# Optimization experiments

Measured on AMD Instinct MI355X. Metric: run time of the kernel, lower is better.

## Reference

```python
import jax, jax.numpy as jnp
import numpy as np

B, N, D, H, F, K, L, V, E, C = 8, 256, 768, 8, 3072, 128, 8, 32, 1024, 2
HD = D // H
LN_EPS = 1e-3  # keras LayerNormalization default epsilon
GAUSS_A = (2.0 * 3.14159) ** 0.5  # constant from source


def _ln(x, g, b):
    m = jnp.mean(x, axis=-1, keepdims=True)
    v = jnp.mean((x - m) ** 2, axis=-1, keepdims=True)
    return (x - m) * jax.lax.rsqrt(v + LN_EPS) * g + b


def _gelu(x):
    return jax.nn.gelu(x, approximate=False)  # keras 'gelu' is exact


def setup_inputs() -> dict:
    key = jax.random.key(0)
    ks = iter(jax.random.split(key, 40))
    s = 0.02
    inp = {
        'dist': jax.random.uniform(next(ks), (B, N, N), jnp.float32) * 10.0,
        'tok_emb': jax.random.normal(next(ks), (V, D), jnp.float32) * s,
        'gmeans': jax.random.uniform(next(ks), (K,), jnp.float32) * 3.0,
        'gstds': jax.random.uniform(next(ks), (K,), jnp.float32) * 3.0,
        'gmul': jnp.ones((E, 1), jnp.float32),
        'gbias': jnp.zeros((E, 1), jnp.float32),
        'gp1w': jax.random.normal(next(ks), (K, K), jnp.float32) * s,
        'gp1b': jnp.zeros((K,), jnp.float32),
        'gp2w': jax.random.normal(next(ks), (K, H), jnp.float32) * s,
        'gp2b': jnp.zeros((H,), jnp.float32),
        'emb_ln_g': jnp.ones((D,), jnp.float32),
        'emb_ln_b': jnp.zeros((D,), jnp.float32),
        'Wq': jax.random.normal(next(ks), (L, D, D), jnp.float32) * s,
        'bq': jnp.zeros((L, D), jnp.float32),
        'Wo': jax.random.normal(next(ks), (L, D, D), jnp.float32) * s,
        'bo': jnp.zeros((L, D), jnp.float32),
        'ln1g': jnp.ones((L, D), jnp.float32),
        'ln1b': jnp.zeros((L, D), jnp.float32),
        'W1': jax.random.normal(next(ks), (L, D, F), jnp.float32) * s,
        'b1': jnp.zeros((L, F), jnp.float32),
        'W2': jax.random.normal(next(ks), (L, F, D), jnp.float32) * s,
        'b2': jnp.zeros((L, D), jnp.float32),
        'ln2g': jnp.ones((L, D), jnp.float32),
        'ln2b': jnp.zeros((L, D), jnp.float32),
        'fin_ln_g': jnp.ones((D,), jnp.float32),
        'fin_ln_b': jnp.zeros((D,), jnp.float32),
        'cls_w1': jax.random.normal(next(ks), (D, D), jnp.float32) * s,
        'cls_b1': jnp.zeros((D,), jnp.float32),
        'cls_w2': jax.random.normal(next(ks), (D, C), jnp.float32) * s,
        'cls_b2': jnp.zeros((C,), jnp.float32),
        'tokens': jax.random.randint(next(ks), (B, N), 0, V, jnp.int64),
        'edge_type': jax.random.randint(next(ks), (B, N, N), 0, E, jnp.int64),
    }
    return inp


def _forward(dist, tok_emb, gmeans, gstds, gmul, gbias, gp1w, gp1b, gp2w, gp2b,
             emb_ln_g, emb_ln_b, Wq, bq, Wo, bo, ln1g, ln1b, W1, b1, W2, b2,
             ln2g, ln2b, fin_ln_g, fin_ln_b, cls_w1, cls_b1, cls_w2, cls_b2,
             tokens, edge_type):
    # --- Gaussian pairwise bias ---
    mul = gmul[edge_type][..., 0]      # (B,N,N)
    add = gbias[edge_type][..., 0]     # (B,N,N)
    y = mul * dist + add               # (B,N,N)
    std = jnp.abs(gstds) + 1e-5        # (K,)
    g = jnp.exp(-0.5 * ((y[..., None] - gmeans) / std) ** 2) / (GAUSS_A * std)  # (B,N,N,K)
    pb = _gelu(g @ gp1w + gp1b) @ gp2w + gp2b   # (B,N,N,H)
    attn_bias = jnp.transpose(pb, (0, 3, 1, 2))  # (B,H,N,N)

    # --- encoder (pre-LN), NB: wq is shared for q/k/v as in source ---
    x = tok_emb[tokens]                # (B,N,D)
    x = _ln(x, emb_ln_g, emb_ln_b)
    scale = 1.0 / np.sqrt(HD).astype(np.float32)

    def split_heads(t):
        return t.reshape(B, N, H, HD).transpose(0, 2, 1, 3)  # (B,H,N,HD)

    for i in range(L):
        r = x
        h = _ln(x, ln1g[i], ln1b[i])
        q = split_heads((h @ Wq[i] + bq[i]) * scale)
        k = split_heads(h @ Wq[i] + bq[i])
        v = split_heads(h @ Wq[i] + bq[i])
        s = jnp.einsum('bhnd,bhmd->bhnm', q, k) + attn_bias
        p = jax.nn.softmax(s, axis=-1)
        o = jnp.einsum('bhnm,bhmd->bhnd', p, v)
        o = o.transpose(0, 2, 1, 3).reshape(B, N, D) @ Wo[i] + bo[i]
        x = o + r
        r = x
        h = _ln(x, ln2g[i], ln2b[i])
        x = _gelu(h @ W1[i] + b1[i]) @ W2[i] + b2[i] + r
    x = _ln(x, fin_ln_g, fin_ln_b)

    # --- classification head on CLS token ---
    cls = x[:, 0, :]
    return _gelu(cls @ cls_w1 + cls_b1) @ cls_w2 + cls_b2  # (B,C)


def reference(dist, tok_emb, gmeans, gstds, gmul, gbias, gp1w, gp1b, gp2w, gp2b,
              emb_ln_g, emb_ln_b, Wq, bq, Wo, bo, ln1g, ln1b, W1, b1, W2, b2,
              ln2g, ln2b, fin_ln_g, fin_ln_b, cls_w1, cls_b1, cls_w2, cls_b2,
              tokens, edge_type):
    return _forward(dist, tok_emb, gmeans, gstds, gmul, gbias, gp1w, gp1b, gp2w,
                    gp2b, emb_ln_g, emb_ln_b, Wq, bq, Wo, bo, ln1g, ln1b, W1, b1,
                    W2, b2, ln2g, ln2b, fin_ln_g, fin_ln_b, cls_w1, cls_b1,
                    cls_w2, cls_b2, tokens, edge_type)
```

## Files before the change

### kernel.cpp

```cpp
#include <hip/hip_runtime.h>
#include <hip/hip_bf16.h>
#include <math.h>


#define DEV_INLINE __device__ __forceinline__

typedef __attribute__((ext_vector_type(8))) short short8v;
typedef __attribute__((ext_vector_type(4))) short short4v;
typedef __attribute__((ext_vector_type(4))) float f32x4;

DEV_INLINE unsigned short f2bf(float f) {
  unsigned u = __float_as_uint(f);
  return (unsigned short)((u + 0x7fffu + ((u >> 16) & 1u)) >> 16);
}
DEV_INLINE unsigned short f2bf_hw(float f) {
  __hip_bfloat16 h = __float2bfloat16(f);
  unsigned short u; __builtin_memcpy(&u, &h, 2); return u;
}
DEV_INLINE float gelu_f(float v) {
  return 0.5f * v * (1.0f + erff(v * 0.70710678118654752f));
}
DEV_INLINE float gelu_tanh(float x) {
  float x2 = x * x;
  float t  = x * fmaf(0.044715f, x2, 1.0f);
  float a  = fminf(2.3022082f * t, 252.0f);
  float e  = __builtin_amdgcn_exp2f(a);
  return x * e * __frcp_rn(e + 1.0f);
}
DEV_INLINE f32x4 zero4() { f32x4 z; z[0]=0.f; z[1]=0.f; z[2]=0.f; z[3]=0.f; return z; }

__global__ __launch_bounds__(256) void k_cast_t(
    const float* __restrict__ W, unsigned short* __restrict__ Wt, int K, int N)
{
  __shared__ float s[64][68];
  const int tid = threadIdx.x;
  const size_t lay = (size_t)blockIdx.z * K * N;
  const int k0 = blockIdx.x * 64, n0 = blockIdx.y * 64;
  const int r = tid >> 4, c4 = (tid & 15) << 2;
  #pragma unroll
  for (int i = 0; i < 4; ++i)
    *(float4*)&s[r + i * 16][c4] =
        *(const float4*)(W + lay + (size_t)(k0 + r + i * 16) * N + n0 + c4);
  __syncthreads();
  const int n = tid & 63, kc = (tid >> 6) << 4;
  short8v v0, v1;
  #pragma unroll
  for (int j = 0; j < 8; ++j) v0[j] = (short)f2bf(s[kc + j][n]);
  #pragma unroll
  for (int j = 0; j < 8; ++j) v1[j] = (short)f2bf(s[kc + 8 + j][n]);
  unsigned short* dst = Wt + lay + (size_t)(n0 + n) * K + k0 + kc;
  *(short8v*)dst = v0;
  *(short8v*)(dst + 8) = v1;
}

__global__ __launch_bounds__(128) void k_cast_g1(
    const float* __restrict__ gp1w, const float* __restrict__ gstds,
    unsigned short* __restrict__ g1t)
{
  const int k = threadIdx.x;
  const int n = blockIdx.x;
  float sd = fabsf(gstds[k]) + 1e-5f;
  float coef = 0.39894268f / sd;
  g1t[n * 128 + k] = f2bf(coef * gp1w[k * 128 + n]);
}

template<int BM, int BN, int EPI>
__global__ __launch_bounds__(256) void k_gemm(
    const unsigned short* __restrict__ A, const unsigned short* __restrict__ Bt,
    const float* __restrict__ bias, const float* __restrict__ res,
    void* __restrict__ C, unsigned short* __restrict__ Vt, int N, int K)
{
  constexpr int MA = BM / 32;
  constexpr int NB = BN / 32;
  __shared__ __align__(16) unsigned short As[BM * 64];
  __shared__ __align__(16) unsigned short Bs[BN * 64];
  const int tid = threadIdx.x;
  const int l = tid & 63;
  const int w = tid >> 6, wr = w >> 1, wc = w & 1;
  const int row0 = blockIdx.x * BM, col0 = blockIdx.y * BN;
  const int NT = K >> 6;

  const int rA = tid >> 3;
  const int cs = (((tid & 7) * 16) ^ ((rA & 7) << 4)) >> 1;
  const unsigned short* pa = A + (size_t)(row0 + rA) * K + (tid & 7) * 8;
  const unsigned short* pb = Bt + (size_t)(col0 + rA) * K + (tid & 7) * 8;

  short8v ra[MA], rb[NB];
  #pragma unroll
  for (int i = 0; i < MA; ++i) ra[i] = *(const short8v*)(pa + (size_t)i * 32 * K);
  #pragma unroll
  for (int i = 0; i < NB; ++i) rb[i] = *(const short8v*)(pb + (size_t)i * 32 * K);

  f32x4 acc[MA][NB];
  #pragma unroll
  for (int mi = 0; mi < MA; ++mi)
    #pragma unroll
    for (int ni = 0; ni < NB; ++ni) acc[mi][ni] = zero4();

  for (int kt = 0; kt < NT; ++kt) {
    #pragma unroll
    for (int i = 0; i < MA; ++i) *(short8v*)&As[(rA + i * 32) * 64 + cs] = ra[i];
    #pragma unroll
    for (int i = 0; i < NB; ++i) *(short8v*)&Bs[(rA + i * 32) * 64 + cs] = rb[i];
    __syncthreads();
    if (kt + 1 < NT) {
      const unsigned short* qa = pa + (size_t)(kt + 1) * 64;
      const unsigned short* qb = pb + (size_t)(kt + 1) * 64;
      #pragma unroll
      for (int i = 0; i < MA; ++i) ra[i] = *(const short8v*)(qa + (size_t)i * 32 * K);
      #pragma unroll
      for (int i = 0; i < NB; ++i) rb[i] = *(const short8v*)(qb + (size_t)i * 32 * K);
    }
    #pragma unroll
    for (int kk = 0; kk < 2; ++kk) {
      short8v af[MA], bf_[NB];
      #pragma unroll
      for (int mi = 0; mi < MA; ++mi) {
        int rw = wr * (BM / 2) + mi * 16 + (l & 15);
        int kb = (kk * 64 + ((l >> 4) << 4)) ^ ((rw & 7) << 4);
        af[mi] = *(const short8v*)&As[rw * 64 + (kb >> 1)];
      }
      #pragma unroll
      for (int ni = 0; ni < NB; ++ni) {
        int rw = wc * (BN / 2) + ni * 16 + (l & 15);
        int kb = (kk * 64 + ((l >> 4) << 4)) ^ ((rw & 7) << 4);
        bf_[ni] = *(const short8v*)&Bs[rw * 64 + (kb >> 1)];
      }
      #pragma unroll
      for (int mi = 0; mi < MA; ++mi)
        #pragma unroll
        for (int ni = 0; ni < NB; ++ni)
          acc[mi][ni] = __builtin_amdgcn_mfma_f32_16x16x32_bf16(
              af[mi], bf_[ni], acc[mi][ni], 0, 0, 0);
    }
    __syncthreads();
  }

  const int cl = l & 15, rg = (l >> 4) << 2;
  #pragma unroll
  for (int mi = 0; mi < MA; ++mi) {
    #pragma unroll
    for (int ni = 0; ni < NB; ++ni) {
      const int colg = col0 + wc * (BN / 2) + ni * 16 + cl;
      const float bv = bias[colg];
      const size_t rbase = (size_t)(row0 + wr * (BM / 2) + mi * 16 + rg);
      if (EPI == 4) {
        short4v pk;
        #pragma unroll
        for (int r = 0; r < 4; ++r) {
          float v = acc[mi][ni][r] + bv;
          unsigned short bb = f2bf(v);
          ((unsigned short*)C)[(rbase + r) * N + colg] = bb;
          pk[r] = (short)bb;
        }
        const int hh = colg / 96, dd = colg - hh * 96;
        const int bb_ = (int)(rbase >> 8), tok = (int)(rbase & 255);
        *(short4v*)(Vt + ((size_t)((bb_ << 3) + hh) * 96 + dd) * 256 + tok) = pk;
      } else {
        #pragma unroll
        for (int r = 0; r < 4; ++r) {
          size_t off = (rbase + r) * N + colg;
          float v = acc[mi][ni][r] + bv;
          if (EPI == 0) ((unsigned short*)C)[off] = f2bf(v);
          if (EPI == 1) ((unsigned short*)C)[off] = f2bf(gelu_f(v));
          if (EPI == 2) ((float*)C)[off] = v + res[off];
        }
      }
    }
  }
}

__global__ __launch_bounds__(256) void k_gauss(
    const float* __restrict__ dist, const int* __restrict__ edge,
    const float* __restrict__ gmul, const float* __restrict__ gbias,
    const float* __restrict__ gmeans, const float* __restrict__ gstds,
    const unsigned short* __restrict__ gp1wt, const float* __restrict__ gp1b,
    const float* __restrict__ gp2w, const float* __restrict__ gp2b,
    float* __restrict__ bias_out)
{
  __shared__ float mean_s[128], c2_s[128], b1s[128];
  __shared__ float b2s[8];
  __shared__ __align__(16) unsigned short w2t[16 * 136];
  __shared__ __align__(16) unsigned short t1[4][2048];
  const int tid = threadIdx.x, l = tid & 63, w = tid >> 6;
  const int pos0 = blockIdx.x * 64;

  if (tid < 128) {
    float sd = fabsf(gstds[tid]) + 1e-5f;
    float inv = 1.0f / sd;
    mean_s[tid] = gmeans[tid];
    c2_s[tid] = -0.72134752f * inv * inv;
    b1s[tid] = gp1b[tid];
  }
  if (tid < 8) b2s[tid] = gp2b[tid];
  for (int i = tid; i < 2048; i += 256) {
    int hh = i & 15, k = i >> 4;
    w2t[hh * 136 + k] = (hh < 8) ? f2bf(gp2w[k * 8 + hh]) : (unsigned short)0;
  }
  __syncthreads();

  const int p = pos0 + w * 16 + (l & 15);
  const int et = edge[p];
  const float y = gmul[et] * dist[p] + gbias[et];

  short8v ga[4];
  #pragma unroll
  for (int ks = 0; ks < 4; ++ks) {
    #pragma unroll
    for (int j = 0; j < 8; ++j) {
      int k = ks * 32 + ((l >> 4) << 3) + j;
      float d = y - mean_s[k];
      ga[ks][j] = (short)f2bf_hw(__builtin_amdgcn_exp2f(c2_s[k] * d * d));
    }
  }
  f32x4 acc[8];
  #pragma unroll
  for (int n = 0; n < 8; ++n) {
    acc[n] = zero4();
    const unsigned short* bp = gp1wt + (size_t)(n * 16 + (l & 15)) * 128 + ((l >> 4) << 3);
    #pragma unroll
    for (int ks = 0; ks < 4; ++ks)
      acc[n] = __builtin_amdgcn_mfma_f32_16x16x32_bf16(
          ga[ks], *(const short8v*)(bp + ks * 32), acc[n], 0, 0, 0);
  }
  unsigned short* tw = t1[w];
  {
    const int rb = (l >> 4) << 2;
    #pragma unroll
    for (int n = 0; n < 8; ++n) {
      int col2 = (n * 16 + (l & 15)) * 2;
      float bb = b1s[n * 16 + (l & 15)];
      #pragma unroll
      for (int r = 0; r < 4; ++r) {
        int row = rb + r;
        int swz = ((row & 3) << 4) ^ ((row >> 2) << 5);
        tw[(row * 256 + (col2 ^ swz)) >> 1] = f2bf_hw(gelu_tanh(acc[n][r] + bb));
      }
    }
  }
  f32x4 o4 = zero4();
  {
    const int row = l & 15;
    const int swz = ((row & 3) << 4) ^ ((row >> 2) << 5);
    #pragma unroll
    for (int ks = 0; ks < 4; ++ks) {
      short8v af = *(const short8v*)&tw[(row * 256 + ((ks * 64 + ((l >> 4) << 4)) ^ swz)) >> 1];
      short8v bf_ = *(const short8v*)&w2t[(l & 15) * 136 + ks * 32 + ((l >> 4) << 3)];
      o4 = __builtin_amdgcn_mfma_f32_16x16x32_bf16(af, bf_, o4, 0, 0, 0);
    }
  }
  const int hh = l & 15;
  if (hh < 8) {
    int b = pos0 >> 16;
    int ij = (pos0 & 65535) + w * 16 + ((l >> 4) << 2);
    float4 vv;
    vv.x = o4[0] + b2s[hh]; vv.y = o4[1] + b2s[hh];
    vv.z = o4[2] + b2s[hh]; vv.w = o4[3] + b2s[hh];
    *(float4*)(bias_out + ((size_t)((b << 3) + hh) << 16) + ij) = vv;
  }
}

__global__ __launch_bounds__(256) void k_embed2(
    const float* __restrict__ emb, const int* __restrict__ tokens,
    const float* __restrict__ eg, const float* __restrict__ eb,
    const float* __restrict__ g1, const float* __restrict__ bp1,
    float* __restrict__ x, unsigned short* __restrict__ h)
{
  __shared__ float red[4], red2[4];
  const int t = threadIdx.x;
  const int row = blockIdx.x;
  const float* xr = emb + (size_t)tokens[row] * 768;
  float v0 = xr[t], v1 = xr[t + 256], v2 = xr[t + 512];
  float s = v0 + v1 + v2;
  #pragma unroll
  for (int o = 32; o; o >>= 1) s += __shfl_down(s, o);
  if ((t & 63) == 0) red[t >> 6] = s;
  __syncthreads();
  float mean = (red[0] + red[1] + red[2] + red[3]) * (1.0f / 768.0f);
  float d0 = v0 - mean, d1 = v1 - mean, d2 = v2 - mean;
  float q = d0 * d0 + d1 * d1 + d2 * d2;
  #pragma unroll
  for (int o = 32; o; o >>= 1) q += __shfl_down(q, o);
  if ((t & 63) == 0) red2[t >> 6] = q;
  __syncthreads();
  float rstd = rsqrtf((red2[0] + red2[1] + red2[2] + red2[3]) * (1.0f / 768.0f) + 1e-3f);
  float* outr = x + (size_t)row * 768;
  float y0 = d0 * rstd * eg[t]       + eb[t];
  float y1 = d1 * rstd * eg[t + 256] + eb[t + 256];
  float y2 = d2 * rstd * eg[t + 512] + eb[t + 512];
  outr[t] = y0; outr[t + 256] = y1; outr[t + 512] = y2;
  __syncthreads();
  s = y0 + y1 + y2;
  #pragma unroll
  for (int o = 32; o; o >>= 1) s += __shfl_down(s, o);
  if ((t & 63) == 0) red[t >> 6] = s;
  __syncthreads();
  mean = (red[0] + red[1] + red[2] + red[3]) * (1.0f / 768.0f);
  d0 = y0 - mean; d1 = y1 - mean; d2 = y2 - mean;
  q = d0 * d0 + d1 * d1 + d2 * d2;
  #pragma unroll
  for (int o = 32; o; o >>= 1) q += __shfl_down(q, o);
  if ((t & 63) == 0) red2[t >> 6] = q;
  __syncthreads();
  rstd = rsqrtf((red2[0] + red2[1] + red2[2] + red2[3]) * (1.0f / 768.0f) + 1e-3f);
  unsigned short* hr = h + (size_t)row * 768;
  hr[t]       = f2bf(d0 * rstd * g1[t]       + bp1[t]);
  hr[t + 256] = f2bf(d1 * rstd * g1[t + 256] + bp1[t + 256]);
  hr[t + 512] = f2bf(d2 * rstd * g1[t + 512] + bp1[t + 512]);
}

__global__ __launch_bounds__(256) void k_ln_bf(
    const float* __restrict__ in, const float* __restrict__ g,
    const float* __restrict__ bp, unsigned short* __restrict__ out)
{
  __shared__ float red[4], red2[4];
  const int t = threadIdx.x;
  const size_t base = (size_t)blockIdx.x * 768;
  const float* xr = in + base;
  float v0 = xr[t], v1 = xr[t + 256], v2 = xr[t + 512];
  float s = v0 + v1 + v2;
  #pragma unroll
  for (int o = 32; o; o >>= 1) s += __shfl_down(s, o);
  if ((t & 63) == 0) red[t >> 6] = s;
  __syncthreads();
  float mean = (red[0] + red[1] + red[2] + red[3]) * (1.0f / 768.0f);
  float d0 = v0 - mean, d1 = v1 - mean, d2 = v2 - mean;
  float q = d0 * d0 + d1 * d1 + d2 * d2;
  #pragma unroll
  for (int o = 32; o; o >>= 1) q += __shfl_down(q, o);
  if ((t & 63) == 0) red2[t >> 6] = q;
  __syncthreads();
  float rstd = rsqrtf((red2[0] + red2[1] + red2[2] + red2[3]) * (1.0f / 768.0f) + 1e-3f);
  unsigned short* outr = out + base;
  outr[t]       = f2bf(d0 * rstd * g[t]       + bp[t]);
  outr[t + 256] = f2bf(d1 * rstd * g[t + 256] + bp[t + 256]);
  outr[t + 512] = f2bf(d2 * rstd * g[t + 512] + bp[t + 512]);
}

__global__ __launch_bounds__(256) void k_attn(
    const unsigned short* __restrict__ P, const unsigned short* __restrict__ Vt,
    const float* __restrict__ bias, unsigned short* __restrict__ O)
{
  __shared__ __align__(16) unsigned short pl[4][4096];
  const int tid = threadIdx.x, l = tid & 63, w = tid >> 6;
  const int i0 = blockIdx.x << 6, bh = blockIdx.y, b = bh >> 3, hh = bh & 7;
  const unsigned short* Pb = P + (size_t)b * 196608 + hh * 96;

  short8v aq[3];
  const int rq = i0 + w * 16 + (l & 15);
  #pragma unroll
  for (int ks = 0; ks < 3; ++ks)
    aq[ks] = *(const short8v*)(Pb + (size_t)rq * 768 + ks * 32 + ((l >> 4) << 3));

  f32x4 acc[16];
  #pragma unroll
  for (int n = 0; n < 16; ++n) {
    acc[n] = zero4();
    const unsigned short* kp = Pb + (size_t)(n * 16 + (l & 15)) * 768 + ((l >> 4) << 3);
    #pragma unroll
    for (int ks = 0; ks < 3; ++ks)
      acc[n] = __builtin_amdgcn_mfma_f32_16x16x32_bf16(
          aq[ks], *(const short8v*)(kp + ks * 32), acc[n], 0, 0, 0);
  }

  const float scale = 0.10206207261596577f;
  float inv[4];
  unsigned short* plw = pl[w];
  const size_t brow = ((size_t)bh * 256 + i0 + w * 16 + ((l >> 4) << 2)) * 256 + (l & 15);
  #pragma unroll
  for (int r = 0; r < 4; ++r) {
    const float* bptr = bias + brow + (size_t)r * 256;
    float m = -1e30f;
    #pragma unroll
    for (int n = 0; n < 16; ++n) {
      float v = acc[n][r] * scale + bptr[n * 16];
      acc[n][r] = v;
      m = fmaxf(m, v);
    }
    m = fmaxf(m, __shfl_xor(m, 1)); m = fmaxf(m, __shfl_xor(m, 2));
    m = fmaxf(m, __shfl_xor(m, 4)); m = fmaxf(m, __shfl_xor(m, 8));
    const int rowL = ((l >> 4) << 2) + r;
    const int swz = ((rowL & 3) << 4) ^ ((rowL >> 2) << 5);
    const int cb = (l & 15) << 1;
    float s = 0.f;
    #pragma unroll
    for (int n = 0; n < 16; ++n) {
      float e = __expf(acc[n][r] - m);
      s += e;
      plw[(rowL * 512 + ((cb + (n << 5)) ^ swz)) >> 1] = f2bf_hw(e);
    }
    s += __shfl_xor(s, 1); s += __shfl_xor(s, 2);
    s += __shfl_xor(s, 4); s += __shfl_xor(s, 8);
    inv[r] = 1.0f / s;
  }

  const int rowA = l & 15;
  const int swzA = ((rowA & 3) << 4) ^ ((rowA >> 2) << 5);
  short8v pa[8];
  #pragma unroll
  for (int ks = 0; ks < 8; ++ks)
    pa[ks] = *(const short8v*)&plw[(rowA * 512 + ((ks * 64 + ((l >> 4) << 4)) ^ swzA)) >> 1];

  unsigned short* Ob = O + ((size_t)b * 256 + i0 + w * 16 + ((l >> 4) << 2)) * 768
                       + hh * 96 + (l & 15);
  #pragma unroll
  for (int n = 0; n < 6; ++n) {
    f32x4 a2 = zero4();
    const unsigned short* vb = Vt + ((size_t)bh * 96 + n * 16 + (l & 15)) * 256 + ((l >> 4) << 3);
    #pragma unroll
    for (int ks = 0; ks < 8; ++ks)
      a2 = __builtin_amdgcn_mfma_f32_16x16x32_bf16(
          pa[ks], *(const short8v*)(vb + ks * 32), a2, 0, 0, 0);
    #pragma unroll
    for (int r = 0; r < 4; ++r)
      Ob[(size_t)r * 768 + n * 16] = f2bf(a2[r] * inv[r]);
  }
}

__global__ __launch_bounds__(256) void k_cls_ln(
    const float* __restrict__ x, const float* __restrict__ fg,
    const float* __restrict__ fb, float* __restrict__ lnb)
{
  __shared__ float red[4], red2[4];
  const int t = threadIdx.x;
  const int b = blockIdx.x;
  const float* xr = x + (size_t)b * 196608;
  float v0 = xr[t], v1 = xr[t + 256], v2 = xr[t + 512];
  float s = v0 + v1 + v2;
  #pragma unroll
  for (int o = 32; o; o >>= 1) s += __shfl_down(s, o);
  if ((t & 63) == 0) red[t >> 6] = s;
  __syncthreads();
  float mean = (red[0] + red[1] + red[2] + red[3]) * (1.0f / 768.0f);
  float d0 = v0 - mean, d1 = v1 - mean, d2 = v2 - mean;
  float q = d0 * d0 + d1 * d1 + d2 * d2;
  #pragma unroll
  for (int o = 32; o; o >>= 1) q += __shfl_down(q, o);
  if ((t & 63) == 0) red2[t >> 6] = q;
  __syncthreads();
  float rstd = rsqrtf((red2[0] + red2[1] + red2[2] + red2[3]) * (1.0f / 768.0f) + 1e-3f);
  float* outr = lnb + b * 768;
  outr[t]       = d0 * rstd * fg[t]       + fb[t];
  outr[t + 256] = d1 * rstd * fg[t + 256] + fb[t + 256];
  outr[t + 512] = d2 * rstd * fg[t + 512] + fb[t + 512];
}

__global__ __launch_bounds__(256) void k_cls_mm(
    const float* __restrict__ lnb, const float* __restrict__ w1,
    const float* __restrict__ b1v, float* __restrict__ t1g)
{
  __shared__ float ln[768];
  const int t = threadIdx.x;
  const int b = blockIdx.x, c0 = blockIdx.y * 256;
  #pragma unroll
  for (int i = 0; i < 3; ++i) ln[t + i * 256] = lnb[b * 768 + t + i * 256];
  __syncthreads();
  float a = b1v[c0 + t];
  for (int d = 0; d < 768; ++d)
    a = fmaf(ln[d], w1[d * 768 + c0 + t], a);
  t1g[b * 768 + c0 + t] = gelu_f(a);
}

__global__ __launch_bounds__(256) void k_cls_out(
    const float* __restrict__ t1g, const float* __restrict__ w2,
    const float* __restrict__ b2v, float* __restrict__ out)
{
  __shared__ float r2[8];
  const int t = threadIdx.x;
  const int b = blockIdx.x;
  float p0 = 0.f, p1 = 0.f;
  #pragma unroll
  for (int oo = 0; oo < 3; ++oo) {
    int d = t + oo * 256;
    float v = t1g[b * 768 + d];
    p0 = fmaf(v, w2[d * 2], p0);
    p1 = fmaf(v, w2[d * 2 + 1], p1);
  }
  #pragma unroll
  for (int o = 32; o; o >>= 1) {
    p0 += __shfl_down(p0, o);
    p1 += __shfl_down(p1, o);
  }
  if ((t & 63) == 0) { r2[t >> 6] = p0; r2[4 + (t >> 6)] = p1; }
  __syncthreads();
  if (t == 0) {
    out[b * 2]     = r2[0] + r2[1] + r2[2] + r2[3] + b2v[0];
    out[b * 2 + 1] = r2[4] + r2[5] + r2[6] + r2[7] + b2v[1];
  }
}

extern "C" void kernel_launch(void* const* d_in, const int* in_sizes, int n_in,
                              void* d_out, int out_size, void* d_ws, size_t ws_size,
                              hipStream_t stream)
{
  const float* dist    = (const float*)d_in[0];
  const float* tok_emb = (const float*)d_in[1];
  const float* gmeans  = (const float*)d_in[2];
  const float* gstds   = (const float*)d_in[3];
  const float* gmul    = (const float*)d_in[4];
  const float* gbias   = (const float*)d_in[5];
  const float* gp1w    = (const float*)d_in[6];
  const float* gp1b    = (const float*)d_in[7];
  const float* gp2w    = (const float*)d_in[8];
  const float* gp2b    = (const float*)d_in[9];
  const float* embg    = (const float*)d_in[10];
  const float* embb    = (const float*)d_in[11];
  const float* Wq      = (const float*)d_in[12];
  const float* bq      = (const float*)d_in[13];
  const float* Wo      = (const float*)d_in[14];
  const float* bo      = (const float*)d_in[15];
  const float* ln1g    = (const float*)d_in[16];
  const float* ln1b    = (const float*)d_in[17];
  const float* W1      = (const float*)d_in[18];
  const float* b1      = (const float*)d_in[19];
  const float* W2      = (const float*)d_in[20];
  const float* b2      = (const float*)d_in[21];
  const float* ln2g    = (const float*)d_in[22];
  const float* ln2b    = (const float*)d_in[23];
  const float* fing    = (const float*)d_in[24];
  const float* finb    = (const float*)d_in[25];
  const float* cw1     = (const float*)d_in[26];
  const float* cb1     = (const float*)d_in[27];
  const float* cw2     = (const float*)d_in[28];
  const float* cb2     = (const float*)d_in[29];
  const int*   tokens  = (const int*)d_in[30];
  const int*   edge    = (const int*)d_in[31];

  float* ws   = (float*)d_ws;
  float* bias = ws;
  float* x    = bias + 4194304;
  float* lnb  = x + 1572864;
  float* t1g  = lnb + 6144;
  unsigned short* hO  = (unsigned short*)(t1g + 6144);
  unsigned short* P   = hO + 1572864;
  unsigned short* Vt  = P + 1572864;
  unsigned short* f1  = Vt + 1572864;
  unsigned short* Wqt = f1 + 6291456;
  unsigned short* Wot = Wqt + 4718592;
  unsigned short* W1t = Wot + 4718592;
  unsigned short* W2t = W1t + 18874368;
  unsigned short* g1t = W2t + 18874368;

  k_cast_g1<<<128, 128, 0, stream>>>(gp1w, gstds, g1t);
  k_gauss<<<8192, 256, 0, stream>>>(dist, edge, gmul, gbias, gmeans, gstds,
                                    g1t, gp1b, gp2w, gp2b, bias);
  k_cast_t<<<dim3(12, 12, 8), 256, 0, stream>>>(Wq, Wqt, 768, 768);
  k_cast_t<<<dim3(12, 12, 8), 256, 0, stream>>>(Wo, Wot, 768, 768);
  k_cast_t<<<dim3(12, 48, 8), 256, 0, stream>>>(W1, W1t, 768, 3072);
  k_cast_t<<<dim3(48, 12, 8), 256, 0, stream>>>(W2, W2t, 3072, 768);
  k_embed2<<<2048, 256, 0, stream>>>(tok_emb, tokens, embg, embb, ln1g, ln1b, x, hO);

  for (int l = 0; l < 8; ++l) {
    k_gemm<64, 64, 4><<<dim3(32, 12), 256, 0, stream>>>(
        hO, Wqt + (size_t)l * 589824, bq + l * 768, nullptr, P, Vt, 768, 768);
    k_attn<<<dim3(4, 64), 256, 0, stream>>>(P, Vt, bias, hO);
    k_gemm<64, 64, 2><<<dim3(32, 12), 256, 0, stream>>>(
        hO, Wot + (size_t)l * 589824, bo + l * 768, x, x, nullptr, 768, 768);
    k_ln_bf<<<2048, 256, 0, stream>>>(x, ln2g + l * 768, ln2b + l * 768, hO);
    k_gemm<128, 128, 1><<<dim3(16, 24), 256, 0, stream>>>(
        hO, W1t + (size_t)l * 2359296, b1 + l * 3072, nullptr, f1, nullptr, 3072, 768);
    k_gemm<64, 64, 2><<<dim3(32, 12), 256, 0, stream>>>(
        f1, W2t + (size_t)l * 2359296, b2 + l * 768, x, x, nullptr, 768, 3072);
    if (l < 7)
      k_ln_bf<<<2048, 256, 0, stream>>>(x, ln1g + (l + 1) * 768,
                                        ln1b + (l + 1) * 768, hO);
  }
  k_cls_ln<<<8, 256, 0, stream>>>(x, fing, finb, lnb);
  k_cls_mm<<<dim3(8, 3), 256, 0, stream>>>(lnb, cw1, cb1, t1g);
  k_cls_out<<<8, 256, 0, stream>>>(t1g, cw2, cb2, (float*)d_out);
}
```

Baseline: 1.153 ms.

## Fuse LayerNorm into GEMM A-loading and store attention bias in bf16

Removes the standalone LayerNorm kernels. The QKV and FFN1 GEMMs now read the fp32 residual directly, compute per-row mean and rstd in a prologue, and normalize plus cast to bf16 while staging A tiles into shared memory. Separately, the Gaussian pair bias is written as bf16 instead of fp32, which halves the traffic the attention kernel reads for it. The cost is redundant row-statistics work in every column block (12 or 24 blocks per row), double-width fp32 A loads, and lower precision in the bias. Row statistics use the E[x^2]-m^2 formula, which is less numerically robust.

New measurement: 1.414 ms. 1.23x slower.

```diff
diff --git a/kernel.cpp b/kernel.cpp
--- a/kernel.cpp
+++ b/kernel.cpp
@@ -16,6 +16,9 @@
 DEV_INLINE unsigned short f2bf_hw(float f) {
   __hip_bfloat16 h = __float2bfloat16(f);
   unsigned short u; __builtin_memcpy(&u, &h, 2); return u;
+}
+DEV_INLINE float bf2f(unsigned short u) {
+  return __uint_as_float(((unsigned)u) << 16);
 }
 DEV_INLINE float gelu_f(float v) {
   return 0.5f * v * (1.0f + erff(v * 0.70710678118654752f));
@@ -64,16 +67,19 @@
   g1t[n * 128 + k] = f2bf(coef * gp1w[k * 128 + n]);
 }
 
-template<int BM, int BN, int EPI>
+template<int BM, int BN, int EPI, int LNA>
 __global__ __launch_bounds__(256) void k_gemm(
-    const unsigned short* __restrict__ A, const unsigned short* __restrict__ Bt,
-    const float* __restrict__ bias, const float* __restrict__ res,
+    const void* __restrict__ Ap, const unsigned short* __restrict__ Bt,
+    const float* __restrict__ bias, const float* __restrict__ lng,
+    const float* __restrict__ lnbv, const float* __restrict__ res,
     void* __restrict__ C, unsigned short* __restrict__ Vt, int N, int K)
 {
   constexpr int MA = BM / 32;
   constexpr int NB = BN / 32;
   __shared__ __align__(16) unsigned short As[BM * 64];
   __shared__ __align__(16) unsigned short Bs[BN * 64];
+  __shared__ float stat_ms[LNA ? BM : 1];
+  __shared__ float stat_rs[LNA ? BM : 1];
   const int tid = threadIdx.x;
   const int l = tid & 63;
   const int w = tid >> 6, wr = w >> 1, wc = w & 1;
@@ -82,15 +88,56 @@
 
   const int rA = tid >> 3;
   const int cs = (((tid & 7) * 16) ^ ((rA & 7) << 4)) >> 1;
-  const unsigned short* pa = A + (size_t)(row0 + rA) * K + (tid & 7) * 8;
-  const unsigned short* pb = Bt + (size_t)(col0 + rA) * K + (tid & 7) * 8;
+  const int kc0 = (tid & 7) * 8;
+
+  const unsigned short* Abf = (const unsigned short*)Ap;
+  const float* Afp = (const float*)Ap;
+  const unsigned short* pb = Bt + (size_t)(col0 + rA) * K + kc0;
 
   short8v ra[MA], rb[NB];
-  #pragma unroll
-  for (int i = 0; i < MA; ++i) ra[i] = *(const short8v*)(pa + (size_t)i * 32 * K);
+  float4 rax[MA], ray[MA];
+  float4 pg0, pg1, pbv0, pbv1;
+  if (LNA) {
+    #pragma unroll
+    for (int i = 0; i < MA; ++i) {
+      const float* p = Afp + (size_t)(row0 + rA + i * 32) * K + kc0;
+      rax[i] = *(const float4*)p;
+      ray[i] = *(const float4*)(p + 4);
+    }
+    pg0 = *(const float4*)(lng + kc0);   pg1 = *(const float4*)(lng + kc0 + 4);
+    pbv0 = *(const float4*)(lnbv + kc0); pbv1 = *(const float4*)(lnbv + kc0 + 4);
+  } else {
+    const unsigned short* pa = Abf + (size_t)(row0 + rA) * K + kc0;
+    #pragma unroll
+    for (int i = 0; i < MA; ++i) ra[i] = *(const short8v*)(pa + (size_t)i * 32 * K);
+  }
   #pragma unroll
   for (int i = 0; i < NB; ++i) rb[i] = *(const short8v*)(pb + (size_t)i * 32 * K);
 
+  if (LNA) {
+    constexpr int TPR = 256 / BM;
+    constexpr int CPT = 768 / TPR;
+    const int sr = tid / TPR, sc = (tid % TPR) * CPT;
+    const float* xr = Afp + (size_t)(row0 + sr) * 768 + sc;
+    float s1 = 0.f, s2 = 0.f;
+    #pragma unroll 8
+    for (int i = 0; i < CPT; i += 4) {
+      float4 v = *(const float4*)(xr + i);
+      s1 += v.x + v.y + v.z + v.w;
+      s2 = fmaf(v.x, v.x, fmaf(v.y, v.y, fmaf(v.z, v.z, fmaf(v.w, v.w, s2))));
+    }
+    s1 += __shfl_xor(s1, 1); s2 += __shfl_xor(s2, 1);
+    if (TPR == 4) { s1 += __shfl_xor(s1, 2); s2 += __shfl_xor(s2, 2); }
+    if ((tid % TPR) == 0) {
+      float m = s1 * (1.0f / 768.0f);
+      float var = s2 * (1.0f / 768.0f) - m * m;
+      float rs = rsqrtf(var + 1e-3f);
+      stat_rs[sr] = rs;
+      stat_ms[sr] = m * rs;
+    }
+    __syncthreads();
+  }
+
   f32x4 acc[MA][NB];
   #pragma unroll
   for (int mi = 0; mi < MA; ++mi)
@@ -98,19 +145,51 @@
     for (int ni = 0; ni < NB; ++ni) acc[mi][ni] = zero4();
 
   for (int kt = 0; kt < NT; ++kt) {
-    #pragma unroll
-    for (int i = 0; i < MA; ++i) *(short8v*)&As[(rA + i * 32) * 64 + cs] = ra[i];
+    if (LNA) {
+      #pragma unroll
+      for (int i = 0; i < MA; ++i) {
+        int r = rA + i * 32;
+        float rs = stat_rs[r], ms = stat_ms[r];
+        short8v o;
+        o[0] = (short)f2bf(fmaf(fmaf(rax[i].x, rs, -ms), pg0.x, pbv0.x));
+        o[1] = (short)f2bf(fmaf(fmaf(rax[i].y, rs, -ms), pg0.y, pbv0.y));
+        o[2] = (short)f2bf(fmaf(fmaf(rax[i].z, rs, -ms), pg0.z, pbv0.z));
+        o[3] = (short)f2bf(fmaf(fmaf(rax[i].w, rs, -ms), pg0.w, pbv0.w));
+        o[4] = (short)f2bf(fmaf(fmaf(ray[i].x, rs, -ms), pg1.x, pbv1.x));
+        o[5] = (short)f2bf(fmaf(fmaf(ray[i].y, rs, -ms), pg1.y, pbv1.y));
+        o[6] = (short)f2bf(fmaf(fmaf(ray[i].z, rs, -ms), pg1.z, pbv1.z));
+        o[7] = (short)f2bf(fmaf(fmaf(ray[i].w, rs, -ms), pg1.w, pbv1.w));
+        *(short8v*)&As[r * 64 + cs] = o;
+      }
+    } else {
+      #pragma unroll
+      for (int i = 0; i < MA; ++i) *(short8v*)&As[(rA + i * 32) * 64 + cs] = ra[i];
+    }
     #pragma unroll
     for (int i = 0; i < NB; ++i) *(short8v*)&Bs[(rA + i * 32) * 64 + cs] = rb[i];
     __syncthreads();
+
     if (kt + 1 < NT) {
-      const unsigned short* qa = pa + (size_t)(kt + 1) * 64;
+      const int kn = (kt + 1) * 64 + kc0;
+      if (LNA) {
+        #pragma unroll
+        for (int i = 0; i < MA; ++i) {
+          const float* p = Afp + (size_t)(row0 + rA + i * 32) * K + kn;
+          rax[i] = *(const float4*)p;
+          ray[i] = *(const float4*)(p + 4);
+        }
+        pg0 = *(const float4*)(lng + kn);   pg1 = *(const float4*)(lng + kn + 4);
+        pbv0 = *(const float4*)(lnbv + kn); pbv1 = *(const float4*)(lnbv + kn + 4);
+      } else {
+        const unsigned short* qa = Abf + (size_t)(row0 + rA) * K + kn;
+        #pragma unroll
+        for (int i = 0; i < MA; ++i) ra[i] = *(const short8v*)(qa + (size_t)i * 32 * K);
+      }
       const unsigned short* qb = pb + (size_t)(kt + 1) * 64;
       #pragma unroll
-      for (int i = 0; i < MA; ++i) ra[i] = *(const short8v*)(qa + (size_t)i * 32 * K);
-      #pragma unroll
       for (int i = 0; i < NB; ++i) rb[i] = *(const short8v*)(qb + (size_t)i * 32 * K);
     }
+
     #pragma unroll
     for (int kk = 0; kk < 2; ++kk) {
       short8v af[MA], bf_[NB];
@@ -176,7 +255,7 @@
     const float* __restrict__ gmeans, const float* __restrict__ gstds,
     const unsigned short* __restrict__ gp1wt, const float* __restrict__ gp1b,
     const float* __restrict__ gp2w, const float* __restrict__ gp2b,
-    float* __restrict__ bias_out)
+    unsigned short* __restrict__ bias_out)
 {
   __shared__ float mean_s[128], c2_s[128], b1s[128];
   __shared__ float b2s[8];
@@ -253,18 +332,17 @@
   if (hh < 8) {
     int b = pos0 >> 16;
     int ij = (pos0 & 65535) + w * 16 + ((l >> 4) << 2);
-    float4 vv;
-    vv.x = o4[0] + b2s[hh]; vv.y = o4[1] + b2s[hh];
-    vv.z = o4[2] + b2s[hh]; vv.w = o4[3] + b2s[hh];
-    *(float4*)(bias_out + ((size_t)((b << 3) + hh) << 16) + ij) = vv;
-  }
-}
-
-__global__ __launch_bounds__(256) void k_embed2(
+    short4v ov;
+    #pragma unroll
+    for (int r = 0; r < 4; ++r) ov[r] = (short)f2bf(o4[r] + b2s[hh]);
+    *(short4v*)(bias_out + (((size_t)((b << 3) + hh)) << 16) + ij) = ov;
+  }
+}
+
+__global__ __launch_bounds__(256) void k_embed_ln(
     const float* __restrict__ emb, const int* __restrict__ tokens,
-    const float* __restrict__ eg, const float* __restrict__ eb,
-    const float* __restrict__ g1, const float* __restrict__ bp1,
-    float* __restrict__ x, unsigned short* __restrict__ h)
+    const float* __restrict__ g, const float* __restrict__ bp,
+    float* __restrict__ out)
 {
   __shared__ float red[4], red2[4];
   const int t = threadIdx.x;
@@ -284,62 +362,15 @@
   if ((t & 63) == 0) red2[t >> 6] = q;
   __syncthreads();
   float rstd = rsqrtf((red2[0] + red2[1] + red2[2] + red2[3]) * (1.0f / 768.0f) + 1e-3f);
-  float* outr = x + (size_t)row * 768;
-  float y0 = d0 * rstd * eg[t]       + eb[t];
-  float y1 = d1 * rstd * eg[t + 256] + eb[t + 256];
-  float y2 = d2 * rstd * eg[t + 512] + eb[t + 512];
-  outr[t] = y0; outr[t + 256] = y1; outr[t + 512] = y2;
-  __syncthreads();
-  s = y0 + y1 + y2;
-  #pragma unroll
-  for (int o = 32; o; o >>= 1) s += __shfl_down(s, o);
-  if ((t & 63) == 0) red[t >> 6] = s;
-  __syncthreads();
-  mean = (red[0] + red[1] + red[2] + red[3]) * (1.0f / 768.0f);
-  d0 = y0 - mean; d1 = y1 - mean; d2 = y2 - mean;
-  q = d0 * d0 + d1 * d1 + d2 * d2;
-  #pragma unroll
-  for (int o = 32; o; o >>= 1) q += __shfl_down(q, o);
-  if ((t & 63) == 0) red2[t >> 6] = q;
-  __syncthreads();
-  rstd = rsqrtf((red2[0] + red2[1] + red2[2] + red2[3]) * (1.0f / 768.0f) + 1e-3f);
-  unsigned short* hr = h + (size_t)row * 768;
-  hr[t]       = f2bf(d0 * rstd * g1[t]       + bp1[t]);
-  hr[t + 256] = f2bf(d1 * rstd * g1[t + 256] + bp1[t + 256]);
-  hr[t + 512] = f2bf(d2 * rstd * g1[t + 512] + bp1[t + 512]);
-}
-
-__global__ __launch_bounds__(256) void k_ln_bf(
-    const float* __restrict__ in, const float* __restrict__ g,
-    const float* __restrict__ bp, unsigned short* __restrict__ out)
-{
-  __shared__ float red[4], red2[4];
-  const int t = threadIdx.x;
-  const size_t base = (size_t)blockIdx.x * 768;
-  const float* xr = in + base;
-  float v0 = xr[t], v1 = xr[t + 256], v2 = xr[t + 512];
-  float s = v0 + v1 + v2;
-  #pragma unroll
-  for (int o = 32; o; o >>= 1) s += __shfl_down(s, o);
-  if ((t & 63) == 0) red[t >> 6] = s;
-  __syncthreads();
-  float mean = (red[0] + red[1] + red[2] + red[3]) * (1.0f / 768.0f);
-  float d0 = v0 - mean, d1 = v1 - mean, d2 = v2 - mean;
-  float q = d0 * d0 + d1 * d1 + d2 * d2;
-  #pragma unroll
-  for (int o = 32; o; o >>= 1) q += __shfl_down(q, o);
-  if ((t & 63) == 0) red2[t >> 6] = q;
-  __syncthreads();
-  float rstd = rsqrtf((red2[0] + red2[1] + red2[2] + red2[3]) * (1.0f / 768.0f) + 1e-3f);
-  unsigned short* outr = out + base;
-  outr[t]       = f2bf(d0 * rstd * g[t]       + bp[t]);
-  outr[t + 256] = f2bf(d1 * rstd * g[t + 256] + bp[t + 256]);
-  outr[t + 512] = f2bf(d2 * rstd * g[t + 512] + bp[t + 512]);
+  float* outr = out + (size_t)row * 768;
+  outr[t]       = d0 * rstd * g[t]       + bp[t];
+  outr[t + 256] = d1 * rstd * g[t + 256] + bp[t + 256];
+  outr[t + 512] = d2 * rstd * g[t + 512] + bp[t + 512];
 }
 
 __global__ __launch_bounds__(256) void k_attn(
     const unsigned short* __restrict__ P, const unsigned short* __restrict__ Vt,
-    const float* __restrict__ bias, unsigned short* __restrict__ O)
+    const unsigned short* __restrict__ bias, unsigned short* __restrict__ O)
 {
   __shared__ __align__(16) unsigned short pl[4][4096];
   const int tid = threadIdx.x, l = tid & 63, w = tid >> 6;
@@ -369,11 +400,11 @@
   const size_t brow = ((size_t)bh * 256 + i0 + w * 16 + ((l >> 4) << 2)) * 256 + (l & 15);
   #pragma unroll
   for (int r = 0; r < 4; ++r) {
-    const float* bptr = bias + brow + (size_t)r * 256;
+    const unsigned short* bptr = bias + brow + (size_t)r * 256;
     float m = -1e30f;
     #pragma unroll
     for (int n = 0; n < 16; ++n) {
-      float v = acc[n][r] * scale + bptr[n * 16];
+      float v = fmaf(acc[n][r], scale, bf2f(bptr[n * 16]));
       acc[n][r] = v;
       m = fmaxf(m, v);
     }
@@ -527,11 +558,11 @@
   const int*   edge    = (const int*)d_in[31];
 
   float* ws   = (float*)d_ws;
-  float* bias = ws;
-  float* x    = bias + 4194304;
+  float* x    = ws;
   float* lnb  = x + 1572864;
   float* t1g  = lnb + 6144;
-  unsigned short* hO  = (unsigned short*)(t1g + 6144);
+  unsigned short* biasb = (unsigned short*)(t1g + 6144);
+  unsigned short* hO  = biasb + 4194304;
   unsigned short* P   = hO + 1572864;
   unsigned short* Vt  = P + 1572864;
   unsigned short* f1  = Vt + 1572864;
@@ -543,27 +574,27 @@
 
   k_cast_g1<<<128, 128, 0, stream>>>(gp1w, gstds, g1t);
   k_gauss<<<8192, 256, 0, stream>>>(dist, edge, gmul, gbias, gmeans, gstds,
-                                    g1t, gp1b, gp2w, gp2b, bias);
+                                    g1t, gp1b, gp2w, gp2b, biasb);
   k_cast_t<<<dim3(12, 12, 8), 256, 0, stream>>>(Wq, Wqt, 768, 768);
   k_cast_t<<<dim3(12, 12, 8), 256, 0, stream>>>(Wo, Wot, 768, 768);
   k_cast_t<<<dim3(12, 48, 8), 256, 0, stream>>>(W1, W1t, 768, 3072);
   k_cast_t<<<dim3(48, 12, 8), 256, 0, stream>>>(W2, W2t, 3072, 768);
-  k_embed2<<<2048, 256, 0, stream>>>(tok_emb, tokens, embg, embb, ln1g, ln1b, x, hO);
+  k_embed_ln<<<2048, 256, 0, stream>>>(tok_emb, tokens, embg, embb, x);
 
   for (int l = 0; l < 8; ++l) {
-    k_gemm<64, 64, 4><<<dim3(32, 12), 256, 0, stream>>>(
-        hO, Wqt + (size_t)l * 589824, bq + l * 768, nullptr, P, Vt, 768, 768);
-    k_attn<<<dim3(4, 64), 256, 0, stream>>>(P, Vt, bias, hO);
-    k_gemm<64, 64, 2><<<dim3(32, 12), 256, 0, stream>>>(
-        hO, Wot + (size_t)l * 589824, bo + l * 768, x, x, nullptr, 768, 768);
-    k_ln_bf<<<2048, 256, 0, stream>>>(x, ln2g + l * 768, ln2b + l * 768, hO);
-    k_gemm<128, 128, 1><<<dim3(16, 24), 256, 0, stream>>>(
-        hO, W1t + (size_t)l * 2359296, b1 + l * 3072, nullptr, f1, nullptr, 3072, 768);
-    k_gemm<64, 64, 2><<<dim3(32, 12), 256, 0, stream>>>(
-        f1, W2t + (size_t)l * 2359296, b2 + l * 768, x, x, nullptr, 768, 3072);
-    if (l < 7)
-      k_ln_bf<<<2048, 256, 0, stream>>>(x, ln1g + (l + 1) * 768,
-                                        ln1b + (l + 1) * 768, hO);
+    k_gemm<64, 64, 4, 1><<<dim3(32, 12), 256, 0, stream>>>(
+        x, Wqt + (size_t)l * 589824, bq + l * 768,
+        ln1g + l * 768, ln1b + l * 768, nullptr, P, Vt, 768, 768);
+    k_attn<<<dim3(4, 64), 256, 0, stream>>>(P, Vt, biasb, hO);
+    k_gemm<64, 64, 2, 0><<<dim3(32, 12), 256, 0, stream>>>(
+        hO, Wot + (size_t)l * 589824, bo + l * 768,
+        nullptr, nullptr, x, x, nullptr, 768, 768);
+    k_gemm<128, 128, 1, 1><<<dim3(16, 24), 256, 0, stream>>>(
+        x, W1t + (size_t)l * 2359296, b1 + l * 3072,
+        ln2g + l * 768, ln2b + l * 768, nullptr, f1, nullptr, 3072, 768);
+    k_gemm<64, 64, 2, 0><<<dim3(32, 12), 256, 0, stream>>>(
+        f1, W2t + (size_t)l * 2359296, b2 + l * 768,
+        nullptr, nullptr, x, x, nullptr, 768, 3072);
   }
   k_cls_ln<<<8, 256, 0, stream>>>(x, fing, finb, lnb);
   k_cls_mm<<<dim3(8, 3), 256, 0, stream>>>(lnb, cw1, cb1, t1g);
```

## Store attention bias in bf16, double gauss work per block, add MFMA priority hints

Applied to the files above, without the earlier changes.

The precomputed graph attention bias (B*H*N*N values) is now written and read as bf16 rather than fp32. This halves the bias traffic that is written once and then read by each of the 8 attention layers. k_gauss now handles 128 positions per block with a two-pass loop, which halves the grid and spreads the per-block shared-memory setup over more work. s_setprio hints are wrapped around the MFMA sections in k_gauss and k_attn. The cost is reduced precision in the bias added to attention scores.

Result: faster. 1.052 ms (-8.8%).

```diff
diff --git a/kernel.cpp b/kernel.cpp
--- a/kernel.cpp
+++ b/kernel.cpp
@@ -16,6 +16,9 @@
 DEV_INLINE unsigned short f2bf_hw(float f) {
   __hip_bfloat16 h = __float2bfloat16(f);
   unsigned short u; __builtin_memcpy(&u, &h, 2); return u;
+}
+DEV_INLINE float bf2f(unsigned short u) {
+  return __uint_as_float(((unsigned)u) << 16);
 }
 DEV_INLINE float gelu_f(float v) {
   return 0.5f * v * (1.0f + erff(v * 0.70710678118654752f));
@@ -176,14 +179,14 @@
     const float* __restrict__ gmeans, const float* __restrict__ gstds,
     const unsigned short* __restrict__ gp1wt, const float* __restrict__ gp1b,
     const float* __restrict__ gp2w, const float* __restrict__ gp2b,
-    float* __restrict__ bias_out)
+    unsigned short* __restrict__ bias_out)
 {
   __shared__ float mean_s[128], c2_s[128], b1s[128];
   __shared__ float b2s[8];
   __shared__ __align__(16) unsigned short w2t[16 * 136];
   __shared__ __align__(16) unsigned short t1[4][2048];
   const int tid = threadIdx.x, l = tid & 63, w = tid >> 6;
-  const int pos0 = blockIdx.x * 64;
+  const int pos0 = blockIdx.x * 128;
 
   if (tid < 128) {
     float sd = fabsf(gstds[tid]) + 1e-5f;
@@ -199,64 +202,71 @@
   }
   __syncthreads();
 
-  const int p = pos0 + w * 16 + (l & 15);
-  const int et = edge[p];
-  const float y = gmul[et] * dist[p] + gbias[et];
-
-  short8v ga[4];
-  #pragma unroll
-  for (int ks = 0; ks < 4; ++ks) {
-    #pragma unroll
-    for (int j = 0; j < 8; ++j) {
-      int k = ks * 32 + ((l >> 4) << 3) + j;
-      float d = y - mean_s[k];
-      ga[ks][j] = (short)f2bf_hw(__builtin_amdgcn_exp2f(c2_s[k] * d * d));
-    }
-  }
-  f32x4 acc[8];
-  #pragma unroll
-  for (int n = 0; n < 8; ++n) {
-    acc[n] = zero4();
-    const unsigned short* bp = gp1wt + (size_t)(n * 16 + (l & 15)) * 128 + ((l >> 4) << 3);
-    #pragma unroll
-    for (int ks = 0; ks < 4; ++ks)
-      acc[n] = __builtin_amdgcn_mfma_f32_16x16x32_bf16(
-          ga[ks], *(const short8v*)(bp + ks * 32), acc[n], 0, 0, 0);
-  }
   unsigned short* tw = t1[w];
-  {
-    const int rb = (l >> 4) << 2;
+  #pragma unroll
+  for (int hb = 0; hb < 2; ++hb) {
+    const int p = pos0 + w * 32 + hb * 16 + (l & 15);
+    const int et = edge[p];
+    const float y = gmul[et] * dist[p] + gbias[et];
+
+    short8v ga[4];
+    #pragma unroll
+    for (int ks = 0; ks < 4; ++ks) {
+      #pragma unroll
+      for (int j = 0; j < 8; ++j) {
+        int k = ks * 32 + ((l >> 4) << 3) + j;
+        float d = y - mean_s[k];
+        ga[ks][j] = (short)f2bf_hw(__builtin_amdgcn_exp2f(c2_s[k] * d * d));
+      }
+    }
+    f32x4 acc[8];
+    __builtin_amdgcn_s_setprio(1);
     #pragma unroll
     for (int n = 0; n < 8; ++n) {
-      int col2 = (n * 16 + (l & 15)) * 2;
-      float bb = b1s[n * 16 + (l & 15)];
-      #pragma unroll
-      for (int r = 0; r < 4; ++r) {
-        int row = rb + r;
-        int swz = ((row & 3) << 4) ^ ((row >> 2) << 5);
-        tw[(row * 256 + (col2 ^ swz)) >> 1] = f2bf_hw(gelu_tanh(acc[n][r] + bb));
+      acc[n] = zero4();
+      const unsigned short* bp = gp1wt + (size_t)(n * 16 + (l & 15)) * 128 + ((l >> 4) << 3);
+      #pragma unroll
+      for (int ks = 0; ks < 4; ++ks)
+        acc[n] = __builtin_amdgcn_mfma_f32_16x16x32_bf16(
+            ga[ks], *(const short8v*)(bp + ks * 32), acc[n], 0, 0, 0);
+    }
+    __builtin_amdgcn_s_setprio(0);
+    {
+      const int rb = (l >> 4) << 2;
+      #pragma unroll
+      for (int n = 0; n < 8; ++n) {
+        int col2 = (n * 16 + (l & 15)) * 2;
+        float bb = b1s[n * 16 + (l & 15)];
+        #pragma unroll
+        for (int r = 0; r < 4; ++r) {
+          int row = rb + r;
+          int swz = ((row & 3) << 4) ^ ((row >> 2) << 5);
+          tw[(row * 256 + (col2 ^ swz)) >> 1] = f2bf_hw(gelu_tanh(acc[n][r] + bb));
+        }
       }
     }
-  }
-  f32x4 o4 = zero4();
-  {
-    const int row = l & 15;
-    const int swz = ((row & 3) << 4) ^ ((row >> 2) << 5);
-    #pragma unroll
-    for (int ks = 0; ks < 4; ++ks) {
-      short8v af = *(const short8v*)&tw[(row * 256 + ((ks * 64 + ((l >> 4) << 4)) ^ swz)) >> 1];
-      short8v bf_ = *(const short8v*)&w2t[(l & 15) * 136 + ks * 32 + ((l >> 4) << 3)];
-      o4 = __builtin_amdgcn_mfma_f32_16x16x32_bf16(af, bf_, o4, 0, 0, 0);
-    }
-  }
-  const int hh = l & 15;
-  if (hh < 8) {
-    int b = pos0 >> 16;
-    int ij = (pos0 & 65535) + w * 16 + ((l >> 4) << 2);
-    float4 vv;
-    vv.x = o4[0] + b2s[hh]; vv.y = o4[1] + b2s[hh];
-    vv.z = o4[2] + b2s[hh]; vv.w = o4[3] + b2s[hh];
-    *(float4*)(bias_out + ((size_t)((b << 3) + hh) << 16) + ij) = vv;
+    f32x4 o4 = zero4();
+    {
+      const int row = l & 15;
+      const int swz = ((row & 3) << 4) ^ ((row >> 2) << 5);
+      __builtin_amdgcn_s_setprio(1);
+      #pragma unroll
+      for (int ks = 0; ks < 4; ++ks) {
+        short8v af = *(const short8v*)&tw[(row * 256 + ((ks * 64 + ((l >> 4) << 4)) ^ swz)) >> 1];
+        short8v bf_ = *(const short8v*)&w2t[(l & 15) * 136 + ks * 32 + ((l >> 4) << 3)];
+        o4 = __builtin_amdgcn_mfma_f32_16x16x32_bf16(af, bf_, o4, 0, 0, 0);
+      }
+      __builtin_amdgcn_s_setprio(0);
+    }
+    const int hh = l & 15;
+    if (hh < 8) {
+      int b = pos0 >> 16;
+      int ij = (pos0 & 65535) + w * 32 + hb * 16 + ((l >> 4) << 2);
+      short4v ov;
+      #pragma unroll
+      for (int r = 0; r < 4; ++r) ov[r] = (short)f2bf(o4[r] + b2s[hh]);
+      *(short4v*)(bias_out + (((size_t)((b << 3) + hh)) << 16) + ij) = ov;
+    }
   }
 }
 
@@ -339,7 +349,7 @@
 
 __global__ __launch_bounds__(256) void k_attn(
     const unsigned short* __restrict__ P, const unsigned short* __restrict__ Vt,
-    const float* __restrict__ bias, unsigned short* __restrict__ O)
+    const unsigned short* __restrict__ bias, unsigned short* __restrict__ O)
 {
   __shared__ __align__(16) unsigned short pl[4][4096];
   const int tid = threadIdx.x, l = tid & 63, w = tid >> 6;
@@ -353,6 +363,7 @@
     aq[ks] = *(const short8v*)(Pb + (size_t)rq * 768 + ks * 32 + ((l >> 4) << 3));
 
   f32x4 acc[16];
+  __builtin_amdgcn_s_setprio(1);
   #pragma unroll
   for (int n = 0; n < 16; ++n) {
     acc[n] = zero4();
@@ -362,6 +373,7 @@
       acc[n] = __builtin_amdgcn_mfma_f32_16x16x32_bf16(
           aq[ks], *(const short8v*)(kp + ks * 32), acc[n], 0, 0, 0);
   }
+  __builtin_amdgcn_s_setprio(0);
 
   const float scale = 0.10206207261596577f;
   float inv[4];
@@ -369,11 +381,11 @@
   const size_t brow = ((size_t)bh * 256 + i0 + w * 16 + ((l >> 4) << 2)) * 256 + (l & 15);
   #pragma unroll
   for (int r = 0; r < 4; ++r) {
-    const float* bptr = bias + brow + (size_t)r * 256;
+    const unsigned short* bptr = bias + brow + (size_t)r * 256;
     float m = -1e30f;
     #pragma unroll
     for (int n = 0; n < 16; ++n) {
-      float v = acc[n][r] * scale + bptr[n * 16];
+      float v = fmaf(acc[n][r], scale, bf2f(bptr[n * 16]));
       acc[n][r] = v;
       m = fmaxf(m, v);
     }
@@ -403,6 +415,7 @@
 
   unsigned short* Ob = O + ((size_t)b * 256 + i0 + w * 16 + ((l >> 4) << 2)) * 768
                        + hh * 96 + (l & 15);
+  __builtin_amdgcn_s_setprio(1);
   #pragma unroll
   for (int n = 0; n < 6; ++n) {
     f32x4 a2 = zero4();
@@ -415,6 +428,7 @@
     for (int r = 0; r < 4; ++r)
       Ob[(size_t)r * 768 + n * 16] = f2bf(a2[r] * inv[r]);
   }
+  __builtin_amdgcn_s_setprio(0);
 }
 
 __global__ __launch_bounds__(256) void k_cls_ln(
@@ -527,11 +541,11 @@
   const int*   edge    = (const int*)d_in[31];
 
   float* ws   = (float*)d_ws;
-  float* bias = ws;
-  float* x    = bias + 4194304;
+  float* x    = ws;
   float* lnb  = x + 1572864;
   float* t1g  = lnb + 6144;
-  unsigned short* hO  = (unsigned short*)(t1g + 6144);
+  unsigned short* biasb = (unsigned short*)(t1g + 6144);
+  unsigned short* hO  = biasb + 4194304;
   unsigned short* P   = hO + 1572864;
   unsigned short* Vt  = P + 1572864;
   unsigned short* f1  = Vt + 1572864;
@@ -542,8 +556,8 @@
   unsigned short* g1t = W2t + 18874368;
 
   k_cast_g1<<<128, 128, 0, stream>>>(gp1w, gstds, g1t);
-  k_gauss<<<8192, 256, 0, stream>>>(dist, edge, gmul, gbias, gmeans, gstds,
-                                    g1t, gp1b, gp2w, gp2b, bias);
+  k_gauss<<<4096, 256, 0, stream>>>(dist, edge, gmul, gbias, gmeans, gstds,
+                                    g1t, gp1b, gp2w, gp2b, biasb);
   k_cast_t<<<dim3(12, 12, 8), 256, 0, stream>>>(Wq, Wqt, 768, 768);
   k_cast_t<<<dim3(12, 12, 8), 256, 0, stream>>>(Wo, Wot, 768, 768);
   k_cast_t<<<dim3(12, 48, 8), 256, 0, stream>>>(W1, W1t, 768, 3072);
@@ -553,7 +567,7 @@
   for (int l = 0; l < 8; ++l) {
     k_gemm<64, 64, 4><<<dim3(32, 12), 256, 0, stream>>>(
         hO, Wqt + (size_t)l * 589824, bq + l * 768, nullptr, P, Vt, 768, 768);
-    k_attn<<<dim3(4, 64), 256, 0, stream>>>(P, Vt, bias, hO);
+    k_attn<<<dim3(4, 64), 256, 0, stream>>>(P, Vt, biasb, hO);
     k_gemm<64, 64, 2><<<dim3(32, 12), 256, 0, stream>>>(
         hO, Wot + (size_t)l * 589824, bo + l * 768, x, x, nullptr, 768, 768);
     k_ln_bf<<<2048, 256, 0, stream>>>(x, ln2g + l * 768, ln2b + l * 768, hO);
```
